# Optimization experiments

Measured on AMD Instinct MI355X. Metric: run time of the kernel, lower is better.

Reference implementation:

```python
import jax, jax.numpy as jnp
import numpy as np

B = 4096
E = 1024   # input_size (embedding)
H = 1024   # hidden_size
C = 1024   # context_vector_size
D = E + H + C  # combined_vector_size


def setup_inputs() -> dict:
    key = jax.random.key(0)
    ks = jax.random.split(key, 20)
    s_gate = 1.0 / np.sqrt(D)
    s_c = 1.0 / np.sqrt(C)
    s_h = 1.0 / np.sqrt(H)
    s_e = 1.0 / np.sqrt(E)
    return {
        "previous_embedded_caption": jax.random.normal(ks[0], (B, E), jnp.float32),
        "previous_hidden_state": jax.random.normal(ks[1], (B, H), jnp.float32),
        "previous_cell_state": jax.random.normal(ks[2], (B, H), jnp.float32),
        "current_context_vector": jax.random.normal(ks[3], (B, C), jnp.float32),
        "Wi": jax.random.uniform(ks[4], (H, D), jnp.float32, -s_gate, s_gate),
        "bi": jax.random.uniform(ks[5], (H,), jnp.float32, -s_gate, s_gate),
        "Wf": jax.random.uniform(ks[6], (H, D), jnp.float32, -s_gate, s_gate),
        "bf": jax.random.uniform(ks[7], (H,), jnp.float32, -s_gate, s_gate),
        "Wo": jax.random.uniform(ks[8], (H, D), jnp.float32, -s_gate, s_gate),
        "bo": jax.random.uniform(ks[9], (H,), jnp.float32, -s_gate, s_gate),
        "Wg": jax.random.uniform(ks[10], (H, D), jnp.float32, -s_gate, s_gate),
        "bg": jax.random.uniform(ks[11], (H,), jnp.float32, -s_gate, s_gate),
        "Wc": jax.random.uniform(ks[12], (E, C), jnp.float32, -s_c, s_c),
        "bc": jax.random.uniform(ks[13], (E,), jnp.float32, -s_c, s_c),
        "Wh": jax.random.uniform(ks[14], (E, H), jnp.float32, -s_h, s_h),
        "bh": jax.random.uniform(ks[15], (E,), jnp.float32, -s_h, s_h),
        "Wp": jax.random.uniform(ks[16], (E, E), jnp.float32, -s_e, s_e),
        "bp": jax.random.uniform(ks[17], (E,), jnp.float32, -s_e, s_e),
    }


def reference(previous_embedded_caption, previous_hidden_state, previous_cell_state,
              current_context_vector, Wi, bi, Wf, bf, Wo, bo, Wg, bg,
              Wc, bc, Wh, bh, Wp, bp):
    # combined vector [B, D]
    combined = jnp.concatenate(
        [previous_embedded_caption, previous_hidden_state, current_context_vector], axis=1)
    i = jax.nn.sigmoid(combined @ Wi.T + bi)
    f = jax.nn.sigmoid(combined @ Wf.T + bf)
    o = jax.nn.sigmoid(combined @ Wo.T + bo)
    g = jnp.tanh(combined @ Wg.T + bg)
    cell = f * previous_cell_state + i * g           # [B, H]
    hidden = o * jnp.tanh(cell)                      # [B, H]
    resid = previous_embedded_caption + (hidden @ Wh.T + bh) + (current_context_vector @ Wc.T + bc)
    prediction = resid @ Wp.T + bp                   # [B, E]
    return (prediction, hidden, cell)
```

## Files before the change

### kernel.cpp

```cpp
#include <hip/hip_runtime.h>
#include <stdint.h>

#define BATCH 4096
#define EHC   1024
#define DCOMB 3072
#define NTOT  ((size_t)BATCH * EHC)
#define WGATE ((size_t)EHC * DCOMB)
#define WSML  ((size_t)EHC * EHC)

#define BK 64

typedef __bf16 bf16x8 __attribute__((ext_vector_type(8)));
typedef float  f32x4  __attribute__((ext_vector_type(4)));

__device__ inline unsigned short f2b(float f) {
    unsigned int x = __float_as_uint(f);
    unsigned int r = (x + 0x7fffu + ((x >> 16) & 1u)) >> 16;
    return (unsigned short)r;
}
__device__ inline float sigmoid_f(float x) { return 1.0f / (1.0f + __expf(-x)); }
__device__ inline float tanh_f(float x) {
    float xa = fminf(fmaxf(x, -15.0f), 15.0f);
    float e = __expf(2.0f * xa);
    return (e - 1.0f) / (e + 1.0f);
}

__device__ inline void load16(const void* g, void* l) {
    __builtin_amdgcn_global_load_lds(
        (const __attribute__((address_space(1))) void*)g,
        (__attribute__((address_space(3))) void*)l, 16, 0, 0);
}

__global__ __launch_bounds__(256)
void cvt_all(const float* __restrict__ s0, const float* __restrict__ s1,
             const float* __restrict__ s2, const float* __restrict__ s3,
             const float* __restrict__ s4, const float* __restrict__ s5,
             const float* __restrict__ s6, const float* __restrict__ s7,
             const float* __restrict__ s8, const float* __restrict__ s9,
             short* __restrict__ dst)
{
    const unsigned b = blockIdx.x;
    const float* src = s0; unsigned st = 0;
    if (b >= 2048)  { src = s1; st = 2048;  }
    if (b >= 4096)  { src = s2; st = 4096;  }
    if (b >= 6144)  { src = s3; st = 6144;  }
    if (b >= 7680)  { src = s4; st = 7680;  }
    if (b >= 9216)  { src = s5; st = 9216;  }
    if (b >= 10752) { src = s6; st = 10752; }
    if (b >= 12288) { src = s7; st = 12288; }
    if (b >= 12800) { src = s8; st = 12800; }
    if (b >= 13312) { src = s9; st = 13312; }
    size_t soff = ((size_t)(b - st) * 2048) + (size_t)threadIdx.x * 8;
    size_t doff = ((size_t)b * 2048) + (size_t)threadIdx.x * 8;
    float4 a = *(const float4*)(src + soff);
    float4 c = *(const float4*)(src + soff + 4);
    uint4 v;
    v.x = (unsigned)f2b(a.x) | ((unsigned)f2b(a.y) << 16);
    v.y = (unsigned)f2b(a.z) | ((unsigned)f2b(a.w) << 16);
    v.z = (unsigned)f2b(c.x) | ((unsigned)f2b(c.y) << 16);
    v.w = (unsigned)f2b(c.z) | ((unsigned)f2b(c.w) << 16);
    *(uint4*)(dst + doff) = v;
}

template <int MODE>
__global__ __launch_bounds__(256, 2)
void gemm_fused(const short* __restrict__ A0, const short* __restrict__ A1,
                const short* __restrict__ A2,
                const short* __restrict__ W0, const short* __restrict__ W1,
                const short* __restrict__ W2, const short* __restrict__ W3,
                const float* __restrict__ b0, const float* __restrict__ b1,
                const float* __restrict__ b2, const float* __restrict__ b3,
                const float* __restrict__ extra,
                void* __restrict__ outv, float* __restrict__ out2,
                short* __restrict__ out3)
{
    constexpr int NG  = (MODE == 1) ? 4 : 1;
    constexpr int BMT = (MODE == 1) ? 128 : 64;
    constexpr int BNT = 64;
    constexpr int MI  = BMT / 32;
    constexpr int NI  = BNT / 32;
    constexpr int AI  = BMT / 32;
    constexpr int BI  = BNT / 32;
    constexpr int WMH = BMT / 2;
    constexpr int BSZ = BNT * BK;

    const int nblk = blockIdx.x;
    const int mblk = blockIdx.y;
    const int tid  = threadIdx.x;
    const int lane = tid & 63;
    const int wave = tid >> 6;
    const int wm = wave >> 1;
    const int wn = wave & 1;
    const int l15 = lane & 15;
    const int l4  = lane >> 4;

    __shared__ short As[BMT * BK];
    __shared__ short Bs[NG * BSZ];

    const int K = (MODE == 1) ? DCOMB : (MODE == 2 ? 2048 : 1024);
    const int wstride = (MODE == 1) ? DCOMB : 1024;
    const int wrowbase = nblk * BNT;

    int aoff[AI], woff[BI];
#pragma unroll
    for (int j = 0; j < AI; j++) {
        int c  = j * 256 + tid;
        int r  = c >> 3;
        int qg = (c & 7) ^ (r & 7);
        aoff[j] = (mblk * BMT + r) * 1024 + qg * 8;
    }
#pragma unroll
    for (int j = 0; j < BI; j++) {
        int c  = j * 256 + tid;
        int r  = c >> 3;
        int qg = (c & 7) ^ (r & 7);
        woff[j] = (wrowbase + r) * wstride + qg * 8;
    }

    int a_ld[2][MI], b_ld[2][NI];
#pragma unroll
    for (int s = 0; s < 2; s++) {
        int q = s * 4 + l4;
#pragma unroll
        for (int i = 0; i < MI; i++) {
            int rowA = wm * WMH + i * 16 + l15;
            a_ld[s][i] = (rowA * 8 + (q ^ (rowA & 7))) * 8;
        }
#pragma unroll
        for (int i = 0; i < NI; i++) {
            int rowB = wn * 32 + i * 16 + l15;
            b_ld[s][i] = (rowB * 8 + (q ^ (rowB & 7))) * 8;
        }
    }

    f32x4 acc[NG][MI][NI];
#pragma unroll
    for (int g = 0; g < NG; g++)
#pragma unroll
        for (int i = 0; i < MI; i++)
#pragma unroll
            for (int j = 0; j < NI; j++) acc[g][i][j] = (f32x4){0.f, 0.f, 0.f, 0.f};

    const int KT = K / BK;
    for (int kt = 0; kt < KT; ++kt) {
        const int k0   = kt * BK;
        const int seg  = (MODE == 3) ? 0 : (k0 >> 10);
        const int acol = k0 & 1023;
        const short* Aseg = (seg == 0) ? A0 : (seg == 1) ? A1 : A2;

        __syncthreads();
#pragma unroll
        for (int j = 0; j < AI; j++)
            load16(Aseg + aoff[j] + acol, &As[(j * 256 + tid) * 8]);
        if (MODE == 1) {
            const short* Wg4[4] = {W0, W1, W2, W3};
#pragma unroll
            for (int g = 0; g < 4; g++)
#pragma unroll
                for (int j = 0; j < BI; j++)
                    load16(Wg4[g] + woff[j] + k0, &Bs[g * BSZ + (j * 256 + tid) * 8]);
        } else {
            const short* Wt = (seg == 0) ? W0 : W1;
#pragma unroll
            for (int j = 0; j < BI; j++)
                load16(Wt + woff[j] + acol, &Bs[(j * 256 + tid) * 8]);
        }
        __syncthreads();

#pragma unroll
        for (int s = 0; s < 2; s++) {
            bf16x8 af[MI];
#pragma unroll
            for (int i = 0; i < MI; i++) af[i] = *(const bf16x8*)(As + a_ld[s][i]);
#pragma unroll
            for (int g = 0; g < NG; g++) {
                bf16x8 bv[NI];
#pragma unroll
                for (int i = 0; i < NI; i++)
                    bv[i] = *(const bf16x8*)(Bs + g * BSZ + b_ld[s][i]);
#pragma unroll
                for (int mi = 0; mi < MI; mi++)
#pragma unroll
                    for (int ni = 0; ni < NI; ni++)
                        acc[g][mi][ni] = __builtin_amdgcn_mfma_f32_16x16x32_bf16(
                            af[mi], bv[ni], acc[g][mi][ni], 0, 0, 0);
            }
        }
    }

#pragma unroll
    for (int ni = 0; ni < NI; ni++) {
        const int col = nblk * BNT + wn * 32 + ni * 16 + l15;
        if (MODE == 1) {
            const float bi_ = b0[col], bf_ = b1[col], bo_ = b2[col], bg_ = b3[col];
#pragma unroll
            for (int mi = 0; mi < MI; mi++) {
#pragma unroll
                for (int r = 0; r < 4; r++) {
                    const size_t row = (size_t)(mblk * BMT + wm * WMH + mi * 16 + l4 * 4 + r);
                    const size_t idx = row * 1024 + col;
                    float ai = fminf(fmaxf(acc[0][mi][ni][r] + bi_, -30.f), 30.f);
                    float af_ = fminf(fmaxf(acc[1][mi][ni][r] + bf_, -30.f), 30.f);
                    float ao = fminf(fmaxf(acc[2][mi][ni][r] + bo_, -30.f), 30.f);
                    float ag = fminf(fmaxf(acc[3][mi][ni][r] + bg_, -30.f), 30.f);
                    float ig = sigmoid_f(ai), fg = sigmoid_f(af_);
                    float og = sigmoid_f(ao), gg = tanh_f(ag);
                    float c = fg * extra[idx] + ig * gg;
                    float h = og * tanh_f(c);
                    ((float*)outv)[idx] = c;
                    out2[idx] = h;
                    out3[idx] = (short)f2b(h);
                }
            }
        } else {
            float bias_v = (MODE == 2) ? (b0[col] + b1[col]) : b0[col];
#pragma unroll
            for (int mi = 0; mi < MI; mi++) {
#pragma unroll
                for (int r = 0; r < 4; r++) {
                    const size_t row = (size_t)(mblk * BMT + wm * WMH + mi * 16 + l4 * 4 + r);
                    const size_t idx = row * 1024 + col;
                    float v = acc[0][mi][ni][r] + bias_v;
                    if (MODE == 2) {
                        v += extra[idx];
                        ((short*)outv)[idx] = (short)f2b(v);
                    } else {
                        ((float*)outv)[idx] = v;
                    }
                }
            }
        }
    }
}

extern "C" void kernel_launch(void* const* d_in, const int* in_sizes, int n_in,
                              void* d_out, int out_size, void* d_ws, size_t ws_size,
                              hipStream_t stream)
{
    const float* emb  = (const float*)d_in[0];
    const float* hid  = (const float*)d_in[1];
    const float* pcel = (const float*)d_in[2];
    const float* ctx  = (const float*)d_in[3];
    const float* Wi = (const float*)d_in[4];   const float* bi = (const float*)d_in[5];
    const float* Wf = (const float*)d_in[6];   const float* bf_ = (const float*)d_in[7];
    const float* Wo = (const float*)d_in[8];   const float* bo = (const float*)d_in[9];
    const float* Wg = (const float*)d_in[10];  const float* bg = (const float*)d_in[11];
    const float* Wc = (const float*)d_in[12];  const float* bc = (const float*)d_in[13];
    const float* Wh = (const float*)d_in[14];  const float* bh = (const float*)d_in[15];
    const float* Wp = (const float*)d_in[16];  const float* bp = (const float*)d_in[17];

    float* out      = (float*)d_out;
    float* pred     = out;
    float* hidden_o = out + NTOT;
    float* cell_o   = out + 2 * NTOT;

    short* ws = (short*)d_ws;
    short* w_emb  = ws;
    short* w_hid  = ws + NTOT;
    short* w_ctx  = ws + 2 * NTOT;
    short* w_Wg4  = ws + 3 * NTOT;
    short* w_Wh   = w_Wg4 + 4 * WGATE;
    short* w_Wc   = w_Wh + WSML;
    short* w_Wp   = w_Wc + WSML;
    short* w_hidb = w_Wp + WSML;
    short* w_res  = w_hidb + NTOT;

    dim3 blk(256, 1, 1);
    const short* np16 = nullptr;
    const float* npf  = nullptr;

    hipLaunchKernelGGL(cvt_all, dim3(13824), blk, 0, stream,
                       emb, hid, ctx, Wi, Wf, Wo, Wg, Wh, Wc, Wp, ws);

    hipLaunchKernelGGL((gemm_fused<1>), dim3(16, 32), blk, 0, stream,
                       w_emb, w_hid, w_ctx,
                       w_Wg4, w_Wg4 + WGATE, w_Wg4 + 2 * WGATE, w_Wg4 + 3 * WGATE,
                       bi, bf_, bo, bg, pcel,
                       (void*)cell_o, hidden_o, w_hidb);
    hipLaunchKernelGGL((gemm_fused<2>), dim3(16, 64), blk, 0, stream,
                       w_hidb, w_ctx, np16, w_Wh, w_Wc, np16, np16,
                       bh, bc, npf, npf, emb, (void*)w_res, (float*)nullptr, (short*)nullptr);
    hipLaunchKernelGGL((gemm_fused<3>), dim3(16, 64), blk, 0, stream,
                       w_res, np16, np16, w_Wp, np16, np16, np16,
                       bp, npf, npf, npf, npf, (void*)pred, (float*)nullptr, (short*)nullptr);
}
```

Baseline: 335.5 us.

## Replace gate GEMM with 512-thread 256x64 tile kernel using staged prefetch

The four-gate LSTM GEMM moves to a new kernel with 8 waves per block and a 256-row by 64-column tile across all four gates. That is a larger tile than the previous 128x64 per block, so each loaded A tile is reused across more columns and gates. Global-to-LDS prefetch of the next K tile is spread across the four gate sub-steps, with partial vmcnt waits, XOR-swizzled LDS layout, and s_setprio around the MFMAs. In exchange it uses 128KB of LDS double buffering, a very large accumulator set, and a 16x16 grid of only 256 blocks, which may limit occupancy and leave compute units underused.

Measured after the change: 336.8 us. No clear change (+0.4%).

```diff
diff --git a/kernel.cpp b/kernel.cpp
--- a/kernel.cpp
+++ b/kernel.cpp
@@ -62,6 +62,174 @@
     *(uint4*)(dst + doff) = v;
 }
 
+__global__ __launch_bounds__(512, 2)
+void gemm_gates8(const short* __restrict__ A0, const short* __restrict__ A1,
+                 const short* __restrict__ A2, const short* __restrict__ W,
+                 const float* __restrict__ b0, const float* __restrict__ b1,
+                 const float* __restrict__ b2, const float* __restrict__ b3,
+                 const float* __restrict__ pcell,
+                 float* __restrict__ cell_o, float* __restrict__ hid_o,
+                 short* __restrict__ hid_b)
+{
+    const int nblk = blockIdx.x;
+    const int mblk = blockIdx.y;
+    const int tid  = threadIdx.x;
+    const int lane = tid & 63;
+    const int wave = tid >> 6;
+    const int wm   = wave >> 1;
+    const int wn   = wave & 1;
+    const int l15  = lane & 15;
+    const int l4   = lane >> 4;
+
+    __shared__ short lds[65536];
+
+    int aoff[2][2], adst[2][2];
+#pragma unroll
+    for (int u = 0; u < 2; u++)
+#pragma unroll
+        for (int j = 0; j < 2; j++) {
+            int ca = u * 1024 + j * 512 + tid;
+            int r  = ca >> 3, q = ca & 7;
+            int qg = q ^ (r & 7);
+            aoff[u][j] = (mblk * 256 + r) * 1024 + qg * 8;
+            adst[u][j] = ca * 8;
+        }
+    int boff[2][2], bdst[2][2];
+#pragma unroll
+    for (int u = 0; u < 2; u++)
+#pragma unroll
+        for (int j = 0; j < 2; j++) {
+            int c2 = j * 512 + tid;
+            int g  = u * 2 + (c2 >> 9);
+            int rb = (c2 >> 3) & 63;
+            int q  = c2 & 7;
+            int qg = q ^ (rb & 7);
+            boff[u][j] = g * (int)WGATE + (nblk * 64 + rb) * 3072 + qg * 8;
+            bdst[u][j] = 16384 + (u * 1024 + c2) * 8;
+        }
+
+    int a_ld[2][4], b_ld[2][2];
+#pragma unroll
+    for (int s = 0; s < 2; s++) {
+        int qf = s * 4 + l4;
+#pragma unroll
+        for (int mi = 0; mi < 4; mi++) {
+            int rowA = wm * 64 + mi * 16 + l15;
+            a_ld[s][mi] = (rowA * 8 + (qf ^ (rowA & 7))) * 8;
+        }
+#pragma unroll
+        for (int ni = 0; ni < 2; ni++) {
+            int rowB = wn * 32 + ni * 16 + l15;
+            b_ld[s][ni] = 16384 + (rowB * 8 + (qf ^ (rowB & 7))) * 8;
+        }
+    }
+
+    f32x4 acc[4][4][2];
+#pragma unroll
+    for (int g = 0; g < 4; g++)
+#pragma unroll
+        for (int mi = 0; mi < 4; mi++)
+#pragma unroll
+            for (int ni = 0; ni < 2; ni++) acc[g][mi][ni] = (f32x4){0.f, 0.f, 0.f, 0.f};
+
+#pragma unroll
+    for (int u = 0; u < 2; u++)
+#pragma unroll
+        for (int j = 0; j < 2; j++)
+            load16(A0 + aoff[u][j], lds + adst[u][j]);
+#pragma unroll
+    for (int u = 0; u < 2; u++)
+#pragma unroll
+        for (int j = 0; j < 2; j++)
+            load16(W + boff[u][j], lds + bdst[u][j]);
+    asm volatile("s_waitcnt vmcnt(2)" ::: "memory");
+    __builtin_amdgcn_s_barrier();
+
+    const int KT = DCOMB / BK;
+#pragma unroll 1
+    for (int t = 0; t < KT; ++t) {
+        const int  P   = (t & 1) * 32768;
+        const bool pf  = (t + 1 < KT);
+        const int  k1  = (t + 1) * 64;
+        const int  Pn  = ((t + 1) & 1) * 32768;
+        const int  ac1 = k1 & 1023;
+        const int  sn  = k1 >> 10;
+        const short* An = (sn == 0) ? A0 : (sn == 1) ? A1 : A2;
+
+        bf16x8 af[2][4];
+#pragma unroll
+        for (int g = 0; g < 4; g++) {
+            if (g == 0) {
+#pragma unroll
+                for (int s = 0; s < 2; s++)
+#pragma unroll
+                    for (int mi = 0; mi < 4; mi++)
+                        af[s][mi] = *(const bf16x8*)(lds + P + a_ld[s][mi]);
+            }
+            bf16x8 bv[2][2];
+#pragma unroll
+            for (int s = 0; s < 2; s++)
+#pragma unroll
+                for (int ni = 0; ni < 2; ni++)
+                    bv[s][ni] = *(const bf16x8*)(lds + P + b_ld[s][ni] + g * 4096);
+
+            if (pf) {
+                if (g < 2) {
+#pragma unroll
+                    for (int j = 0; j < 2; j++)
+                        load16(An + aoff[g][j] + ac1, lds + Pn + adst[g][j]);
+                } else {
+#pragma unroll
+                    for (int j = 0; j < 2; j++)
+                        load16(W + boff[g - 2][j] + k1, lds + Pn + bdst[g - 2][j]);
+                }
+            }
+
+            if (g == 1) asm volatile("s_waitcnt vmcnt(4)" ::: "memory");
+            if (g == 3) asm volatile("s_waitcnt vmcnt(2)" ::: "memory");
+
+            __builtin_amdgcn_s_barrier();
+            asm volatile("s_waitcnt lgkmcnt(0)" ::: "memory");
+            __builtin_amdgcn_s_setprio(1);
+#pragma unroll
+            for (int s = 0; s < 2; s++)
+#pragma unroll
+                for (int mi = 0; mi < 4; mi++)
+#pragma unroll
+                    for (int ni = 0; ni < 2; ni++)
+                        acc[g][mi][ni] = __builtin_amdgcn_mfma_f32_16x16x32_bf16(
+                            af[s][mi], bv[s][ni], acc[g][mi][ni], 0, 0, 0);
+            __builtin_amdgcn_s_setprio(0);
+            __builtin_amdgcn_s_barrier();
+        }
+    }
+
+#pragma unroll
+    for (int ni = 0; ni < 2; ni++) {
+        const int col = nblk * 64 + wn * 32 + ni * 16 + l15;
+        const float bi_ = b0[col], bf_ = b1[col], bo_ = b2[col], bg_ = b3[col];
+#pragma unroll
+        for (int mi = 0; mi < 4; mi++) {
+#pragma unroll
+            for (int r = 0; r < 4; r++) {
+                const size_t row = (size_t)(mblk * 256 + wm * 64 + mi * 16 + l4 * 4 + r);
+                const size_t idx = row * 1024 + col;
+                float ai  = fminf(fmaxf(acc[0][mi][ni][r] + bi_, -30.f), 30.f);
+                float af_ = fminf(fmaxf(acc[1][mi][ni][r] + bf_, -30.f), 30.f);
+                float ao  = fminf(fmaxf(acc[2][mi][ni][r] + bo_, -30.f), 30.f);
+                float ag  = fminf(fmaxf(acc[3][mi][ni][r] + bg_, -30.f), 30.f);
+                float ig = sigmoid_f(ai), fg = sigmoid_f(af_);
+                float og = sigmoid_f(ao), gg = tanh_f(ag);
+                float c = fg * pcell[idx] + ig * gg;
+                float h = og * tanh_f(c);
+                cell_o[idx] = c;
+                hid_o[idx]  = h;
+                hid_b[idx]  = (short)f2b(h);
+            }
+        }
+    }
+}
+
 template <int MODE>
 __global__ __launch_bounds__(256, 2)
 void gemm_fused(const short* __restrict__ A0, const short* __restrict__ A1,
@@ -272,11 +440,10 @@
     hipLaunchKernelGGL(cvt_all, dim3(13824), blk, 0, stream,
                        emb, hid, ctx, Wi, Wf, Wo, Wg, Wh, Wc, Wp, ws);
 
-    hipLaunchKernelGGL((gemm_fused<1>), dim3(16, 32), blk, 0, stream,
-                       w_emb, w_hid, w_ctx,
-                       w_Wg4, w_Wg4 + WGATE, w_Wg4 + 2 * WGATE, w_Wg4 + 3 * WGATE,
+    hipLaunchKernelGGL(gemm_gates8, dim3(16, 16), dim3(512, 1, 1), 0, stream,
+                       w_emb, w_hid, w_ctx, w_Wg4,
                        bi, bf_, bo, bg, pcel,
-                       (void*)cell_o, hidden_o, w_hidb);
+                       cell_o, hidden_o, w_hidb);
     hipLaunchKernelGGL((gemm_fused<2>), dim3(16, 64), blk, 0, stream,
                        w_hidb, w_ctx, np16, w_Wh, w_Wc, np16, np16,
                        bh, bc, npf, npf, emb, (void*)w_res, (float*)nullptr, (short*)nullptr);
```
